# Kernel optimization log

Measured on AMD Instinct MI355X. Metric: run time of the kernel, lower is better.

## Reference

```python
import jax, jax.numpy as jnp
import numpy as np

NSAMPLE = 3  # three_nn default
EPS = 1e-10
CLAMP = 10.0


def setup_inputs() -> dict:
    key = jax.random.key(0)
    k1, k2, k3 = jax.random.split(key, 3)
    B, C, N = 4, 3, 8192
    pos1 = jax.random.normal(k1, (B, C, N), dtype=jnp.float32)
    pos2 = jax.random.normal(k2, (B, C, N), dtype=jnp.float32)
    flow1 = jax.random.normal(k3, (B, C, N), dtype=jnp.float32) * 0.1
    return {"pos1": pos1, "pos2": pos2, "flow1": flow1}


def reference(pos1, pos2, flow1):
    # pos1, flow1: [B,3,N1]; pos2: [B,3,N2]
    pos1_to_2 = pos1 + flow1                       # warped source points [B,3,N1]
    q = jnp.transpose(pos2, (0, 2, 1))             # queries  [B,N2,3]
    k = jnp.transpose(pos1_to_2, (0, 2, 1))        # database [B,N1,3]

    # brute-force 3-NN: squared distances [B,N2,N1]
    d2 = (jnp.sum(q * q, axis=-1, keepdims=True)
          - 2.0 * jnp.einsum('bqc,bnc->bqn', q, k)
          + jnp.sum(k * k, axis=-1)[:, None, :])
    _, knn_idx = jax.lax.top_k(-d2, NSAMPLE)       # [B,N2,NSAMPLE] into N1

    # gather neighbor coords: [B,N2,NSAMPLE,3]
    grouped_pts = jax.vmap(lambda pts, ii: pts[ii])(k, knn_idx)
    diff = grouped_pts - q[:, :, None, :]
    dist = jnp.maximum(jnp.linalg.norm(diff, axis=-1), EPS)  # [B,N2,NSAMPLE]
    inv = 1.0 / dist
    weight = inv / jnp.sum(inv, axis=-1, keepdims=True)      # [B,N2,NSAMPLE]

    # gather neighbor flows and do inverse-distance-weighted average
    flow_t = jnp.transpose(flow1, (0, 2, 1))                 # [B,N1,3]
    grouped_flow = jax.vmap(lambda f, ii: f[ii])(flow_t, knn_idx)  # [B,N2,NSAMPLE,3]
    flow2 = jnp.sum(weight[..., None] * grouped_flow, axis=2)      # [B,N2,3]

    warped = pos2 - jnp.transpose(flow2, (0, 2, 1))          # [B,3,N2]
    return jnp.clip(warped, -CLAMP, CLAMP)
```

## Files before the change

### kernel.cpp

```cpp
#include <hip/hip_runtime.h>
#include <math.h>


#define BB 4
#define NN 8192
#define NC 30
#define NCELLS (NC * NC * NC)
#define NCT (BB * NCELLS)
#define GRID_R 3.3f
#define GRID_INVH (1.0f / 0.22f)
#define D3_THR (0.44f * 0.44f * 0.999f)
#define EPB 1024
#define SB 106
#define NZ4 ((NCT + 4) / 4)

typedef unsigned long long u64;

__device__ __forceinline__ int cell_of(float x) {
  int c = (int)floorf((x + GRID_R) * GRID_INVH);
  return min(max(c, 0), NC - 1);
}

__device__ __forceinline__ void merge3(u64& a0, u64& a1, u64& a2,
                                       u64 b0, u64 b1, u64 b2) {
  const u64 lo0 = a0 < b0 ? a0 : b0;
  const u64 hi0 = a0 < b0 ? b0 : a0;
  const u64 lo1 = a1 < b1 ? a1 : b1;
  const u64 lo2 = a2 < b2 ? a2 : b2;
  const u64 o1 = hi0 < lo1 ? hi0 : lo1;
  const u64 t = hi0 < lo1 ? lo1 : hi0;
  a0 = lo0;
  a1 = o1;
  a2 = t < lo2 ? t : lo2;
}

__device__ __forceinline__ void insert3(u64& s0, u64& s1, u64& s2, u64 key) {
  const bool c0 = key < s0;
  const bool c1 = key < s1;
  const bool c2 = key < s2;
  s2 = c1 ? s1 : (c2 ? key : s2);
  s1 = c0 ? s0 : (c1 ? key : s1);
  s0 = c0 ? key : s0;
}

__device__ __forceinline__ void wave_merge3(u64& s0, u64& s1, u64& s2) {
#pragma unroll
  for (int mask = 32; mask >= 1; mask >>= 1) {
    const u64 b0 = __shfl_xor(s0, mask, 64);
    const u64 b1 = __shfl_xor(s1, mask, 64);
    const u64 b2 = __shfl_xor(s2, mask, 64);
    merge3(s0, s1, s2, b0, b1, b2);
  }
}

__device__ __forceinline__ void idw_out(int b, int qn, float qx, float qy,
                                        float qz, u64 s0, u64 s1, u64 s2,
                                        const float* __restrict__ P1,
                                        const float* __restrict__ F1,
                                        float* __restrict__ out) {
  const int idxs[3] = {(int)(unsigned)s0 & (NN - 1),
                       (int)(unsigned)s1 & (NN - 1),
                       (int)(unsigned)s2 & (NN - 1)};
  float w[3], gfx[3], gfy[3], gfz[3];
  float wsumv = 0.0f;
#pragma unroll
  for (int r = 0; r < 3; ++r) {
    const int idx = idxs[r];
    const float fx = F1[idx], fy = F1[NN + idx], fz = F1[2 * NN + idx];
    const float kx = P1[idx] + fx;
    const float ky = P1[NN + idx] + fy;
    const float kz = P1[2 * NN + idx] + fz;
    const float dx = kx - qx, dy = ky - qy, dz = kz - qz;
    float d = sqrtf(dx * dx + dy * dy + dz * dz);
    d = fmaxf(d, 1e-10f);
    const float inv = 1.0f / d;
    w[r] = inv; wsumv += inv;
    gfx[r] = fx; gfy[r] = fy; gfz[r] = fz;
  }
  const float invw = 1.0f / wsumv;
  float ox = 0.0f, oy = 0.0f, oz = 0.0f;
#pragma unroll
  for (int r = 0; r < 3; ++r) {
    const float ww = w[r] * invw;
    ox = fmaf(ww, gfx[r], ox);
    oy = fmaf(ww, gfy[r], oy);
    oz = fmaf(ww, gfz[r], oz);
  }
  ox = qx - ox; oy = qy - oy; oz = qz - oz;
  ox = fminf(fmaxf(ox, -10.0f), 10.0f);
  oy = fminf(fmaxf(oy, -10.0f), 10.0f);
  oz = fminf(fmaxf(oz, -10.0f), 10.0f);
  float* o = out + (size_t)b * 3 * NN;
  o[qn] = ox;
  o[NN + qn] = oy;
  o[2 * NN + qn] = oz;
}

__global__ __launch_bounds__(256) void k_zero(int4* __restrict__ p) {
  const int i = blockIdx.x * 256 + threadIdx.x;
  if (i < NZ4) p[i] = make_int4(0, 0, 0, 0);
}

__global__ __launch_bounds__(256) void k_count(const float* __restrict__ p1,
                                               const float* __restrict__ f1,
                                               int* __restrict__ counts) {
  const int gid = blockIdx.x * 256 + threadIdx.x;
  const int b = gid >> 13, n = gid & (NN - 1);
  const float* P = p1 + (size_t)b * 3 * NN;
  const float* F = f1 + (size_t)b * 3 * NN;
  const float x = P[n] + F[n];
  const float y = P[NN + n] + F[NN + n];
  const float z = P[2 * NN + n] + F[2 * NN + n];
  const int cid = (cell_of(z) * NC + cell_of(y)) * NC + cell_of(x);
  atomicAdd(&counts[b * NCELLS + cid], 1);
}

__global__ __launch_bounds__(256) void k_scan1(int* __restrict__ counts,
                                               int* __restrict__ offs,
                                               int* __restrict__ partials) {
  __shared__ int wsums[4];
  const int tid = threadIdx.x, lane = tid & 63, wav = tid >> 6;
  const int c = blockIdx.x * EPB + tid * 4;
  int4 v = make_int4(0, 0, 0, 0);
  if (c < NCT) {
    v = *reinterpret_cast<const int4*>(counts + c);
    *reinterpret_cast<int4*>(counts + c) = make_int4(0, 0, 0, 0);
  }
  const int sum4 = v.x + v.y + v.z + v.w;
  int incl = sum4;
  for (int off = 1; off < 64; off <<= 1) {
    const int t = __shfl_up(incl, off, 64);
    incl += (lane >= off) ? t : 0;
  }
  if (lane == 63) wsums[wav] = incl;
  __syncthreads();
  int wbase = 0;
#pragma unroll
  for (int w = 0; w < 4; ++w) wbase += (w < wav) ? wsums[w] : 0;
  const int excl = wbase + incl - sum4;
  if (c < NCT) {
    int4 e;
    e.x = excl;
    e.y = excl + v.x;
    e.z = e.y + v.y;
    e.w = e.z + v.z;
    *reinterpret_cast<int4*>(offs + c) = e;
  }
  if (tid == 255) partials[blockIdx.x] = wbase + incl;
}

__global__ __launch_bounds__(128) void k_scan2(int* __restrict__ partials) {
  __shared__ int w0sum;
  const int t = threadIdx.x, lane = t & 63, wav = t >> 6;
  const int v = (t < SB) ? partials[t] : 0;
  int incl = v;
  for (int off = 1; off < 64; off <<= 1) {
    const int u = __shfl_up(incl, off, 64);
    incl += (lane >= off) ? u : 0;
  }
  if (t == 63) w0sum = incl;
  __syncthreads();
  const int base = wav ? w0sum : 0;
  if (t < SB) partials[t] = base + incl - v;
}

__global__ __launch_bounds__(256) void k_apply(int* __restrict__ offs,
                                               const int* __restrict__ partials) {
  const int base = partials[blockIdx.x];
  const int c = blockIdx.x * EPB + threadIdx.x * 4;
  if (c < NCT) {
    int4 v = *reinterpret_cast<const int4*>(offs + c);
    v.x += base; v.y += base; v.z += base; v.w += base;
    *reinterpret_cast<int4*>(offs + c) = v;
  }
  if (blockIdx.x == 0 && threadIdx.x == 0) offs[NCT] = BB * NN;
}

__global__ __launch_bounds__(256) void k_scatter(const float* __restrict__ p1,
                                                 const float* __restrict__ f1,
                                                 int* __restrict__ counts,
                                                 const int* __restrict__ offs,
                                                 float4* __restrict__ csr) {
  const int gid = blockIdx.x * 256 + threadIdx.x;
  const int b = gid >> 13, n = gid & (NN - 1);
  const float* P = p1 + (size_t)b * 3 * NN;
  const float* F = f1 + (size_t)b * 3 * NN;
  const float x = P[n] + F[n];
  const float y = P[NN + n] + F[NN + n];
  const float z = P[2 * NN + n] + F[2 * NN + n];
  const int cid = (cell_of(z) * NC + cell_of(y)) * NC + cell_of(x);
  const int g = b * NCELLS + cid;
  const int rank = atomicAdd(&counts[g], 1);
  csr[offs[g] + rank] = make_float4(x, y, z, __int_as_float(n));
}

__device__ __forceinline__ void col_range(int c, int qcy, int qcz, int cb,
                                          int gxl, int span,
                                          const int* __restrict__ offs,
                                          int& st, int& en) {
  const int dzi = (c * 205) >> 10;
  const int gz = qcz + dzi - 2;
  const int gy = qcy + (c - dzi * 5) - 2;
  st = 0; en = 0;
  if (((unsigned)gz < NC) & ((unsigned)gy < NC)) {
    const int ia = cb + (gz * NC + gy) * NC + gxl;
    st = offs[ia];
    en = offs[ia + span];
  }
}

__device__ __forceinline__ void scan_col(int st, int en,
                                         const float4* __restrict__ csr,
                                         float qx, float qy, float qz,
                                         u64& s0, u64& s1, u64& s2) {
  int j = st;
  for (; j + 2 <= en; j += 2) {
    const float4 a = csr[j];
    const float4 c = csr[j + 1];
    {
      const float dx = a.x - qx, dy = a.y - qy, dz = a.z - qz;
      const float d2 = fmaf(dx, dx, fmaf(dy, dy, dz * dz));
      insert3(s0, s1, s2,
              ((u64)__float_as_uint(d2) << 32) | (unsigned)__float_as_uint(a.w));
    }
    {
      const float dx = c.x - qx, dy = c.y - qy, dz = c.z - qz;
      const float d2 = fmaf(dx, dx, fmaf(dy, dy, dz * dz));
      insert3(s0, s1, s2,
              ((u64)__float_as_uint(d2) << 32) | (unsigned)__float_as_uint(c.w));
    }
  }
  if (j < en) {
    const float4 a = csr[j];
    const float dx = a.x - qx, dy = a.y - qy, dz = a.z - qz;
    const float d2 = fmaf(dx, dx, fmaf(dy, dy, dz * dz));
    insert3(s0, s1, s2,
            ((u64)__float_as_uint(d2) << 32) | (unsigned)__float_as_uint(a.w));
  }
}

__global__ __launch_bounds__(256) void k_query(const float* __restrict__ p1,
                                               const float* __restrict__ p2,
                                               const float* __restrict__ f1,
                                               const int* __restrict__ offs,
                                               const float4* __restrict__ csr,
                                               float* __restrict__ out,
                                               int* __restrict__ fbcnt,
                                               int* __restrict__ fbq) {
  const int gtid = blockIdx.x * 256 + threadIdx.x;
  const int qid = gtid >> 3;
  const int r = gtid & 7;
  const int b = qid >> 13;
  const int qn = qid & (NN - 1);
  const float* P1 = p1 + (size_t)b * 3 * NN;
  const float* P2 = p2 + (size_t)b * 3 * NN;
  const float* F1 = f1 + (size_t)b * 3 * NN;

  const float qx = P2[qn], qy = P2[NN + qn], qz = P2[2 * NN + qn];
  const bool oor = !(fabsf(qx) < GRID_R && fabsf(qy) < GRID_R && fabsf(qz) < GRID_R);

  u64 s0 = ~0ULL, s1 = ~0ULL, s2 = ~0ULL;

  if (!oor) {
    const int qcx = cell_of(qx), qcy = cell_of(qy), qcz = cell_of(qz);
    const int gxl = max(qcx - 2, 0);
    const int span = min(qcx + 2, NC - 1) - gxl + 1;
    const int cb = b * NCELLS;

    int st0, en0, st1, en1, st2, en2, st3 = 0, en3 = 0;
    col_range(r, qcy, qcz, cb, gxl, span, offs, st0, en0);
    col_range(r + 8, qcy, qcz, cb, gxl, span, offs, st1, en1);
    col_range(r + 16, qcy, qcz, cb, gxl, span, offs, st2, en2);
    if (r == 0) col_range(24, qcy, qcz, cb, gxl, span, offs, st3, en3);

    scan_col(st0, en0, csr, qx, qy, qz, s0, s1, s2);
    scan_col(st1, en1, csr, qx, qy, qz, s0, s1, s2);
    scan_col(st2, en2, csr, qx, qy, qz, s0, s1, s2);
    scan_col(st3, en3, csr, qx, qy, qz, s0, s1, s2);
  }

#pragma unroll
  for (int mask = 1; mask <= 4; mask <<= 1) {
    const u64 b0 = __shfl_xor(s0, mask, 64);
    const u64 b1 = __shfl_xor(s1, mask, 64);
    const u64 b2 = __shfl_xor(s2, mask, 64);
    merge3(s0, s1, s2, b0, b1, b2);
  }

  if (r == 0) {
    const float d3 = __uint_as_float((unsigned)(s2 >> 32));
    const bool ok = !oor && (d3 <= D3_THR);
    if (!ok) {
      const int slot = atomicAdd(&fbcnt[b], 1);
      fbq[b * NN + slot] = qn;
    } else {
      idw_out(b, qn, qx, qy, qz, s0, s1, s2, P1, F1, out);
    }
  }
}

__device__ __forceinline__ float sbcast(float v) {
  return __int_as_float(__builtin_amdgcn_readfirstlane(__float_as_int(v)));
}

__global__ __launch_bounds__(256) void k_fallback(const float* __restrict__ p1,
                                                  const float* __restrict__ p2,
                                                  const float* __restrict__ f1,
                                                  const int* __restrict__ fbcnt,
                                                  const int* __restrict__ fbq,
                                                  float* __restrict__ out) {
  __shared__ float4 tile[1024];
  const int b = blockIdx.y;
  const int nfb = fbcnt[b];
  const int tid = threadIdx.x, lane = tid & 63, wav = tid >> 6;
  const float* P1 = p1 + (size_t)b * 3 * NN;
  const float* P2 = p2 + (size_t)b * 3 * NN;
  const float* F1 = f1 + (size_t)b * 3 * NN;
  const int* q = fbq + b * NN;

  for (int base = blockIdx.x * 8; base < nfb; base += gridDim.x * 8) {
    const int myq = base + wav * 2;
    const bool v0 = myq < nfb;
    const bool v1 = myq + 1 < nfb;
    int qn0 = v0 ? q[myq] : 0;
    int qn1 = v1 ? q[myq + 1] : 0;
    qn0 = __builtin_amdgcn_readfirstlane(qn0);
    qn1 = __builtin_amdgcn_readfirstlane(qn1);
    const float q0x = sbcast(P2[qn0]), q0y = sbcast(P2[NN + qn0]), q0z = sbcast(P2[2 * NN + qn0]);
    const float q1x = sbcast(P2[qn1]), q1y = sbcast(P2[NN + qn1]), q1z = sbcast(P2[2 * NN + qn1]);

    u64 a0 = ~0ULL, a1 = ~0ULL, a2 = ~0ULL;
    u64 c0 = ~0ULL, c1 = ~0ULL, c2 = ~0ULL;

    for (int t = 0; t < NN / 1024; ++t) {
      __syncthreads();
#pragma unroll
      for (int k = 0; k < 4; ++k) {
        const int j = k * 256 + tid;
        const int g = t * 1024 + j;
        const float x = P1[g] + F1[g];
        const float y = P1[NN + g] + F1[NN + g];
        const float z = P1[2 * NN + g] + F1[2 * NN + g];
        tile[j] = make_float4(x, y, z, __int_as_float(g));
      }
      __syncthreads();
#pragma unroll 4
      for (int j = 0; j < 16; ++j) {
        const float4 pt = tile[j * 64 + lane];
        const unsigned idx = (unsigned)__float_as_int(pt.w);
        {
          const float dx = pt.x - q0x, dy = pt.y - q0y, dz = pt.z - q0z;
          const float d2 = fmaf(dx, dx, fmaf(dy, dy, dz * dz));
          insert3(a0, a1, a2, ((u64)__float_as_uint(d2) << 32) | idx);
        }
        {
          const float dx = pt.x - q1x, dy = pt.y - q1y, dz = pt.z - q1z;
          const float d2 = fmaf(dx, dx, fmaf(dy, dy, dz * dz));
          insert3(c0, c1, c2, ((u64)__float_as_uint(d2) << 32) | idx);
        }
      }
    }

    wave_merge3(a0, a1, a2);
    wave_merge3(c0, c1, c2);
    if (lane == 0 && v0) idw_out(b, qn0, q0x, q0y, q0z, a0, a1, a2, P1, F1, out);
    if (lane == 0 && v1) idw_out(b, qn1, q1x, q1y, q1z, c0, c1, c2, P1, F1, out);
  }
}

extern "C" void kernel_launch(void* const* d_in, const int* in_sizes, int n_in,
                              void* d_out, int out_size, void* d_ws, size_t ws_size,
                              hipStream_t stream) {
  const float* pos1 = (const float*)d_in[0];
  const float* pos2 = (const float*)d_in[1];
  const float* flow1 = (const float*)d_in[2];
  float* out = (float*)d_out;

  char* ws = (char*)d_ws;
  int* counts = (int*)ws;
  int* fbcnt = counts + NCT;
  size_t offs_off = (((size_t)NCT + 4) * 4 + 15) & ~(size_t)15;
  int* offs = (int*)(ws + offs_off);
  size_t part_off = (offs_off + ((size_t)NCT + 1) * 4 + 15) & ~(size_t)15;
  int* partials = (int*)(ws + part_off);
  size_t fbq_off = (part_off + (size_t)SB * 4 + 15) & ~(size_t)15;
  int* fbq = (int*)(ws + fbq_off);
  size_t csr_off = (fbq_off + (size_t)BB * NN * 4 + 15) & ~(size_t)15;
  float4* csr = (float4*)(ws + csr_off);

  k_zero<<<dim3((NZ4 + 255) / 256), dim3(256), 0, stream>>>((int4*)counts);
  k_count<<<dim3(BB * NN / 256), dim3(256), 0, stream>>>(pos1, flow1, counts);
  k_scan1<<<dim3(SB), dim3(256), 0, stream>>>(counts, offs, partials);
  k_scan2<<<dim3(1), dim3(128), 0, stream>>>(partials);
  k_apply<<<dim3(SB), dim3(256), 0, stream>>>(offs, partials);
  k_scatter<<<dim3(BB * NN / 256), dim3(256), 0, stream>>>(pos1, flow1, counts, offs, csr);
  k_query<<<dim3(BB * NN * 8 / 256), dim3(256), 0, stream>>>(pos1, pos2, flow1, offs, csr, out, fbcnt, fbq);
  k_fallback<<<dim3(64, BB), dim3(256), 0, stream>>>(pos1, pos2, flow1, fbcnt, fbq, out);
}
```

Measured before the change: 78.18 us.

## Fuse scan kernels, widen query to 16 lanes, restructure fallback per block

Merges the single-block partial scan and the apply kernel into one finalize kernel, where each block sums its preceding partials directly, removing one launch. The query kernel now gives each query 16 threads instead of 8, so each lane scans at most two of the 25 neighbour columns, and the column scan is unrolled by four. The fallback kernel drops the shared-memory tile and syncs: each block now handles two queries across all 256 threads and reduces per-wave results through shared memory, with more blocks launched. This trades more threads, one extra shuffle level and block-level reductions for more parallelism and fewer launches.

```diff
diff --git a/kernel.cpp b/kernel.cpp
--- a/kernel.cpp
+++ b/kernel.cpp
@@ -149,31 +149,27 @@
   if (tid == 255) partials[blockIdx.x] = wbase + incl;
 }
 
-__global__ __launch_bounds__(128) void k_scan2(int* __restrict__ partials) {
-  __shared__ int w0sum;
-  const int t = threadIdx.x, lane = t & 63, wav = t >> 6;
-  const int v = (t < SB) ? partials[t] : 0;
-  int incl = v;
-  for (int off = 1; off < 64; off <<= 1) {
-    const int u = __shfl_up(incl, off, 64);
-    incl += (lane >= off) ? u : 0;
-  }
-  if (t == 63) w0sum = incl;
+__global__ __launch_bounds__(256) void k_finalize(int* __restrict__ offs,
+                                                  const int* __restrict__ partials) {
+  __shared__ int sbase;
+  const int tid = threadIdx.x, lane = tid & 63;
+  const int bid = blockIdx.x;
+  if (tid < 64) {
+    int v = 0;
+    if (lane < bid) v = partials[lane];
+    if (lane + 64 < bid) v += partials[lane + 64];
+    for (int off = 32; off >= 1; off >>= 1) v += __shfl_down(v, off, 64);
+    if (lane == 0) sbase = v;
+  }
   __syncthreads();
-  const int base = wav ? w0sum : 0;
-  if (t < SB) partials[t] = base + incl - v;
-}
-
-__global__ __launch_bounds__(256) void k_apply(int* __restrict__ offs,
-                                               const int* __restrict__ partials) {
-  const int base = partials[blockIdx.x];
-  const int c = blockIdx.x * EPB + threadIdx.x * 4;
+  const int base = sbase;
+  const int c = bid * EPB + tid * 4;
   if (c < NCT) {
     int4 v = *reinterpret_cast<const int4*>(offs + c);
     v.x += base; v.y += base; v.z += base; v.w += base;
     *reinterpret_cast<int4*>(offs + c) = v;
   }
-  if (blockIdx.x == 0 && threadIdx.x == 0) offs[NCT] = BB * NN;
+  if (bid == 0 && tid == 0) offs[NCT] = BB * NN;
 }
 
 __global__ __launch_bounds__(256) void k_scatter(const float* __restrict__ p1,
@@ -209,33 +205,32 @@
   }
 }
 
+__device__ __forceinline__ void cand1(const float4& a, float qx, float qy,
+                                      float qz, u64& s0, u64& s1, u64& s2) {
+  const float dx = a.x - qx, dy = a.y - qy, dz = a.z - qz;
+  const float d2 = fmaf(dx, dx, fmaf(dy, dy, dz * dz));
+  insert3(s0, s1, s2,
+          ((u64)__float_as_uint(d2) << 32) | (unsigned)__float_as_uint(a.w));
+}
+
 __device__ __forceinline__ void scan_col(int st, int en,
                                          const float4* __restrict__ csr,
                                          float qx, float qy, float qz,
                                          u64& s0, u64& s1, u64& s2) {
   int j = st;
-  for (; j + 2 <= en; j += 2) {
+  for (; j + 4 <= en; j += 4) {
     const float4 a = csr[j];
-    const float4 c = csr[j + 1];
-    {
-      const float dx = a.x - qx, dy = a.y - qy, dz = a.z - qz;
-      const float d2 = fmaf(dx, dx, fmaf(dy, dy, dz * dz));
-      insert3(s0, s1, s2,
-              ((u64)__float_as_uint(d2) << 32) | (unsigned)__float_as_uint(a.w));
-    }
-    {
-      const float dx = c.x - qx, dy = c.y - qy, dz = c.z - qz;
-      const float d2 = fmaf(dx, dx, fmaf(dy, dy, dz * dz));
-      insert3(s0, s1, s2,
-              ((u64)__float_as_uint(d2) << 32) | (unsigned)__float_as_uint(c.w));
-    }
-  }
-  if (j < en) {
+    const float4 b = csr[j + 1];
+    const float4 c = csr[j + 2];
+    const float4 d = csr[j + 3];
+    cand1(a, qx, qy, qz, s0, s1, s2);
+    cand1(b, qx, qy, qz, s0, s1, s2);
+    cand1(c, qx, qy, qz, s0, s1, s2);
+    cand1(d, qx, qy, qz, s0, s1, s2);
+  }
+  for (; j < en; ++j) {
     const float4 a = csr[j];
-    const float dx = a.x - qx, dy = a.y - qy, dz = a.z - qz;
-    const float d2 = fmaf(dx, dx, fmaf(dy, dy, dz * dz));
-    insert3(s0, s1, s2,
-            ((u64)__float_as_uint(d2) << 32) | (unsigned)__float_as_uint(a.w));
+    cand1(a, qx, qy, qz, s0, s1, s2);
   }
 }
 
@@ -248,8 +243,8 @@
                                                int* __restrict__ fbcnt,
                                                int* __restrict__ fbq) {
   const int gtid = blockIdx.x * 256 + threadIdx.x;
-  const int qid = gtid >> 3;
-  const int r = gtid & 7;
+  const int qid = gtid >> 4;
+  const int r = gtid & 15;
   const int b = qid >> 13;
   const int qn = qid & (NN - 1);
   const float* P1 = p1 + (size_t)b * 3 * NN;
@@ -267,20 +262,16 @@
     const int span = min(qcx + 2, NC - 1) - gxl + 1;
     const int cb = b * NCELLS;
 
-    int st0, en0, st1, en1, st2, en2, st3 = 0, en3 = 0;
+    int st0, en0, st1 = 0, en1 = 0;
     col_range(r, qcy, qcz, cb, gxl, span, offs, st0, en0);
-    col_range(r + 8, qcy, qcz, cb, gxl, span, offs, st1, en1);
-    col_range(r + 16, qcy, qcz, cb, gxl, span, offs, st2, en2);
-    if (r == 0) col_range(24, qcy, qcz, cb, gxl, span, offs, st3, en3);
+    if (r < 9) col_range(r + 16, qcy, qcz, cb, gxl, span, offs, st1, en1);
 
     scan_col(st0, en0, csr, qx, qy, qz, s0, s1, s2);
     scan_col(st1, en1, csr, qx, qy, qz, s0, s1, s2);
-    scan_col(st2, en2, csr, qx, qy, qz, s0, s1, s2);
-    scan_col(st3, en3, csr, qx, qy, qz, s0, s1, s2);
-  }
-
-#pragma unroll
-  for (int mask = 1; mask <= 4; mask <<= 1) {
+  }
+
+#pragma unroll
+  for (int mask = 1; mask <= 8; mask <<= 1) {
     const u64 b0 = __shfl_xor(s0, mask, 64);
     const u64 b1 = __shfl_xor(s1, mask, 64);
     const u64 b2 = __shfl_xor(s2, mask, 64);
@@ -299,17 +290,14 @@
   }
 }
 
-__device__ __forceinline__ float sbcast(float v) {
-  return __int_as_float(__builtin_amdgcn_readfirstlane(__float_as_int(v)));
-}
-
 __global__ __launch_bounds__(256) void k_fallback(const float* __restrict__ p1,
                                                   const float* __restrict__ p2,
                                                   const float* __restrict__ f1,
                                                   const int* __restrict__ fbcnt,
                                                   const int* __restrict__ fbq,
                                                   float* __restrict__ out) {
-  __shared__ float4 tile[1024];
+  __shared__ u64 redA[4][3];
+  __shared__ u64 redC[4][3];
   const int b = blockIdx.y;
   const int nfb = fbcnt[b];
   const int tid = threadIdx.x, lane = tid & 63, wav = tid >> 6;
@@ -318,53 +306,62 @@
   const float* F1 = f1 + (size_t)b * 3 * NN;
   const int* q = fbq + b * NN;
 
-  for (int base = blockIdx.x * 8; base < nfb; base += gridDim.x * 8) {
-    const int myq = base + wav * 2;
-    const bool v0 = myq < nfb;
-    const bool v1 = myq + 1 < nfb;
-    int qn0 = v0 ? q[myq] : 0;
-    int qn1 = v1 ? q[myq + 1] : 0;
-    qn0 = __builtin_amdgcn_readfirstlane(qn0);
-    qn1 = __builtin_amdgcn_readfirstlane(qn1);
-    const float q0x = sbcast(P2[qn0]), q0y = sbcast(P2[NN + qn0]), q0z = sbcast(P2[2 * NN + qn0]);
-    const float q1x = sbcast(P2[qn1]), q1y = sbcast(P2[NN + qn1]), q1z = sbcast(P2[2 * NN + qn1]);
+  for (int base = blockIdx.x * 2; base < nfb; base += gridDim.x * 2) {
+    const bool v1 = base + 1 < nfb;
+    const int qn0 = q[base] & (NN - 1);
+    const int qn1 = (v1 ? q[base + 1] : q[base]) & (NN - 1);
+    const float q0x = P2[qn0], q0y = P2[NN + qn0], q0z = P2[2 * NN + qn0];
+    const float q1x = P2[qn1], q1y = P2[NN + qn1], q1z = P2[2 * NN + qn1];
 
     u64 a0 = ~0ULL, a1 = ~0ULL, a2 = ~0ULL;
     u64 c0 = ~0ULL, c1 = ~0ULL, c2 = ~0ULL;
 
-    for (int t = 0; t < NN / 1024; ++t) {
-      __syncthreads();
+    for (int g0 = 0; g0 < NN; g0 += 1024) {
+      const int g = g0 + tid;
+      float xs[4], ys[4], zs[4];
 #pragma unroll
       for (int k = 0; k < 4; ++k) {
-        const int j = k * 256 + tid;
-        const int g = t * 1024 + j;
-        const float x = P1[g] + F1[g];
-        const float y = P1[NN + g] + F1[NN + g];
-        const float z = P1[2 * NN + g] + F1[2 * NN + g];
-        tile[j] = make_float4(x, y, z, __int_as_float(g));
+        const int gg = g + k * 256;
+        xs[k] = P1[gg] + F1[gg];
+        ys[k] = P1[NN + gg] + F1[NN + gg];
+        zs[k] = P1[2 * NN + gg] + F1[2 * NN + gg];
       }
-      __syncthreads();
-#pragma unroll 4
-      for (int j = 0; j < 16; ++j) {
-        const float4 pt = tile[j * 64 + lane];
-        const unsigned idx = (unsigned)__float_as_int(pt.w);
+#pragma unroll
+      for (int k = 0; k < 4; ++k) {
+        const unsigned gg = (unsigned)(g + k * 256);
         {
-          const float dx = pt.x - q0x, dy = pt.y - q0y, dz = pt.z - q0z;
+          const float dx = xs[k] - q0x, dy = ys[k] - q0y, dz = zs[k] - q0z;
           const float d2 = fmaf(dx, dx, fmaf(dy, dy, dz * dz));
-          insert3(a0, a1, a2, ((u64)__float_as_uint(d2) << 32) | idx);
+          insert3(a0, a1, a2, ((u64)__float_as_uint(d2) << 32) | gg);
         }
         {
-          const float dx = pt.x - q1x, dy = pt.y - q1y, dz = pt.z - q1z;
+          const float dx = xs[k] - q1x, dy = ys[k] - q1y, dz = zs[k] - q1z;
           const float d2 = fmaf(dx, dx, fmaf(dy, dy, dz * dz));
-          insert3(c0, c1, c2, ((u64)__float_as_uint(d2) << 32) | idx);
+          insert3(c0, c1, c2, ((u64)__float_as_uint(d2) << 32) | gg);
         }
       }
     }
 
     wave_merge3(a0, a1, a2);
     wave_merge3(c0, c1, c2);
-    if (lane == 0 && v0) idw_out(b, qn0, q0x, q0y, q0z, a0, a1, a2, P1, F1, out);
-    if (lane == 0 && v1) idw_out(b, qn1, q1x, q1y, q1z, c0, c1, c2, P1, F1, out);
+    if (lane == 0) {
+      redA[wav][0] = a0; redA[wav][1] = a1; redA[wav][2] = a2;
+      redC[wav][0] = c0; redC[wav][1] = c1; redC[wav][2] = c2;
+    }
+    __syncthreads();
+    if (tid == 0) {
+      u64 m0 = redA[0][0], m1 = redA[0][1], m2 = redA[0][2];
+#pragma unroll
+      for (int w = 1; w < 4; ++w) merge3(m0, m1, m2, redA[w][0], redA[w][1], redA[w][2]);
+      idw_out(b, qn0, q0x, q0y, q0z, m0, m1, m2, P1, F1, out);
+    }
+    if (tid == 1 && v1) {
+      u64 m0 = redC[0][0], m1 = redC[0][1], m2 = redC[0][2];
+#pragma unroll
+      for (int w = 1; w < 4; ++w) merge3(m0, m1, m2, redC[w][0], redC[w][1], redC[w][2]);
+      idw_out(b, qn1, q1x, q1y, q1z, m0, m1, m2, P1, F1, out);
+    }
+    __syncthreads();
   }
 }
 
@@ -391,9 +388,8 @@
   k_zero<<<dim3((NZ4 + 255) / 256), dim3(256), 0, stream>>>((int4*)counts);
   k_count<<<dim3(BB * NN / 256), dim3(256), 0, stream>>>(pos1, flow1, counts);
   k_scan1<<<dim3(SB), dim3(256), 0, stream>>>(counts, offs, partials);
-  k_scan2<<<dim3(1), dim3(128), 0, stream>>>(partials);
-  k_apply<<<dim3(SB), dim3(256), 0, stream>>>(offs, partials);
+  k_finalize<<<dim3(SB), dim3(256), 0, stream>>>(offs, partials);
   k_scatter<<<dim3(BB * NN / 256), dim3(256), 0, stream>>>(pos1, flow1, counts, offs, csr);
-  k_query<<<dim3(BB * NN * 8 / 256), dim3(256), 0, stream>>>(pos1, pos2, flow1, offs, csr, out, fbcnt, fbq);
-  k_fallback<<<dim3(64, BB), dim3(256), 0, stream>>>(pos1, pos2, flow1, fbcnt, fbq, out);
-}
+  k_query<<<dim3(BB * NN * 16 / 256), dim3(256), 0, stream>>>(pos1, pos2, flow1, offs, csr, out, fbcnt, fbq);
+  k_fallback<<<dim3(128, BB), dim3(256), 0, stream>>>(pos1, pos2, flow1, fbcnt, fbq, out);
+}
```

Measured after the change: 70.97 us. 9.2% less time.
